# Kernel tuning notes

Hardware: AMD Instinct MI355X
Metric: run time of the kernel (lower is better)

The kernel has to match this reference:

```python
import jax, jax.numpy as jnp
import numpy as np

B, N, D, H = 1, 4096, 1024, 16
HD = D // H  # head_dim = 64


def setup_inputs() -> dict:
    key = jax.random.key(0)
    ks = jax.random.split(key, 5)
    s = 0.02
    return {
        "x": jax.random.normal(ks[0], (B, N, D), dtype=jnp.float32),
        "Wq": jax.random.normal(ks[1], (D, D), dtype=jnp.float32) * s,
        "Wk": jax.random.normal(ks[2], (D, D), dtype=jnp.float32) * s,
        "Wv": jax.random.normal(ks[3], (D, D), dtype=jnp.float32) * s,
        "Wo": jax.random.normal(ks[4], (D, D), dtype=jnp.float32) * s,
        "bo": jnp.zeros((D,), dtype=jnp.float32),
    }


def reference(x, Wq, Wk, Wv, Wo, bo):
    b, n, d = x.shape
    # QKV projections -> [b, h, n, hd]
    def proj(W):
        return jnp.einsum("bnd,de->bne", x, W).reshape(b, n, H, HD).transpose(0, 2, 1, 3)
    q, k, v = proj(Wq), proj(Wk), proj(Wv)
    # Scores [b, h, n, n] with causal mask (matches masked_fill with triu(diag=1))
    scores = jnp.einsum("bhqd,bhkd->bhqk", q, k)
    causal = jnp.tril(jnp.ones((n, n), dtype=bool))
    scores = jnp.where(causal, scores, -jnp.inf)
    attn = jax.nn.softmax(scores / jnp.sqrt(jnp.float32(HD)), axis=-1)
    # dropout p=0.0 -> identity
    ctx = jnp.einsum("bhqk,bhkd->bhqd", attn, v)
    ctx = ctx.transpose(0, 2, 1, 3).reshape(b, n, d)
    return jnp.einsum("bnd,de->bne", ctx, Wo) + bo
```

## Files before the change

### kernel.cpp

```cpp
#include <hip/hip_runtime.h>


#define N_TOK 4096
#define DMODEL 1024
#define NH 16
#define HDIM 64

typedef __bf16 bf16x8 __attribute__((ext_vector_type(8)));
typedef __bf16 bf16x2v __attribute__((ext_vector_type(2)));
typedef short short4v __attribute__((ext_vector_type(4)));
typedef unsigned int uint2v __attribute__((ext_vector_type(2)));
typedef float f32x4 __attribute__((ext_vector_type(4)));

__device__ __forceinline__ unsigned short f2bf(float f) {
  unsigned u = __builtin_bit_cast(unsigned, f);
  u += 0x7FFFu + ((u >> 16) & 1u);
  return (unsigned short)(u >> 16);
}

__device__ __forceinline__ float bf2f(unsigned short u) {
  unsigned x = (unsigned)u << 16;
  return __builtin_bit_cast(float, x);
}

__device__ __forceinline__ unsigned pack2bf(float f0, float f1) {
  unsigned a = __builtin_bit_cast(unsigned, f0);
  unsigned b = __builtin_bit_cast(unsigned, f1);
  a += 0x7FFFu + ((a >> 16) & 1u);
  b += 0x7FFFu + ((b >> 16) & 1u);
  return (a >> 16) | (b & 0xFFFF0000u);
}

__device__ __forceinline__ unsigned packpk(float f0, float f1) {
#if defined(__HIP_DEVICE_COMPILE__) && __has_builtin(__builtin_amdgcn_cvt_pk_bf16_f32)
  bf16x2v r = __builtin_amdgcn_cvt_pk_bf16_f32(f0, f1);
  return __builtin_bit_cast(unsigned, r);
#else
  return pack2bf(f0, f1);
#endif
}

__device__ __forceinline__ float fast_exp2(float x) {
#if defined(__HIP_DEVICE_COMPILE__)
#if __has_builtin(__builtin_amdgcn_exp2f)
  return __builtin_amdgcn_exp2f(x);
#else
  float r;
  asm("v_exp_f32 %0, %1" : "=v"(r) : "v"(x));
  return r;
#endif
#else
  return exp2f(x);
#endif
}

__device__ __forceinline__ f32x4 mfma16x16x16(short4v a, short4v b, f32x4 c) {
#if defined(__HIP_DEVICE_COMPILE__)
#if __has_builtin(__builtin_amdgcn_mfma_f32_16x16x16bf16_1k)
  return __builtin_amdgcn_mfma_f32_16x16x16bf16_1k(a, b, c, 0, 0, 0);
#else
  asm volatile("v_mfma_f32_16x16x16_bf16 %0, %1, %2, %0\n\ts_nop 7\n\ts_nop 1"
               : "+v"(c) : "v"(a), "v"(b));
  return c;
#endif
#else
  return c;
#endif
}

__device__ __forceinline__ void gll16(const unsigned short* g, unsigned short* l) {
#if defined(__HIP_DEVICE_COMPILE__)
  __builtin_amdgcn_global_load_lds((const __attribute__((address_space(1))) void*)g,
                                   (__attribute__((address_space(3))) void*)l, 16, 0, 0);
#endif
}

__global__ __launch_bounds__(256) void prep_kernel(
    const float* __restrict__ x, unsigned short* __restrict__ xb,
    const float* __restrict__ Wq, const float* __restrict__ Wk,
    const float* __restrict__ Wv, const float* __restrict__ Wo,
    unsigned short* __restrict__ Wqt, unsigned short* __restrict__ Wkt,
    unsigned short* __restrict__ Wvt, unsigned short* __restrict__ Wot) {
  const int bx = blockIdx.x;
  if (bx < 4096) {
    const int i = (bx * 256 + threadIdx.x) * 4;
    float4 v = *(const float4*)(x + i);
    ushort4 o;
    o.x = f2bf(v.x); o.y = f2bf(v.y); o.z = f2bf(v.z); o.w = f2bf(v.w);
    *(ushort4*)(xb + i) = o;
    return;
  }
  __shared__ float t[32][33];
  const int r = bx - 4096;
  const int z = r >> 10, rem = r & 1023;
  const int by = rem >> 5, bxx = rem & 31;
  const float* src;
  unsigned short* dst;
  switch (z) {
    case 0: src = Wq; dst = Wqt; break;
    case 1: src = Wk; dst = Wkt; break;
    case 2: src = Wv; dst = Wvt; break;
    default: src = Wo; dst = Wot; break;
  }
  const int tx = threadIdx.x & 31, ty = threadIdx.x >> 5;
  const int xx = bxx * 32 + tx;
  const int y0 = by * 32;
#pragma unroll
  for (int i = 0; i < 32; i += 8) t[ty + i][tx] = src[(y0 + ty + i) * DMODEL + xx];
  __syncthreads();
  const int ox = by * 32 + tx;
  const int oy0 = bxx * 32;
#pragma unroll
  for (int i = 0; i < 32; i += 8) dst[(oy0 + ty + i) * DMODEL + ox] = f2bf(t[tx][ty + i]);
}

__global__ __launch_bounds__(256) void gemm_qkv_kernel(
    const unsigned short* __restrict__ xb,
    const unsigned short* __restrict__ Wqt, const unsigned short* __restrict__ Wkt,
    const unsigned short* __restrict__ Wvt,
    unsigned short* __restrict__ Qg, unsigned short* __restrict__ Kg,
    unsigned short* __restrict__ Vtg) {
  __shared__ unsigned short As[128 * 32];
  __shared__ unsigned short Bs[128 * 32];
  __shared__ unsigned short Tt[64 * 132];
  const int z = blockIdx.z;
  const unsigned short* Bmat = (z == 0) ? Wqt : ((z == 1) ? Wkt : Wvt);
  const int tid = threadIdx.x, lane = tid & 63, wv = tid >> 6;
  const int quad = lane >> 4, l15 = lane & 15;
  const int wm = wv >> 1, wn = wv & 1;
  const int tm0 = blockIdx.y * 128, tn0 = blockIdx.x * 128;
  const int lrow = lane >> 2, lcol = (lane & 3) * 8;
  const f32x4 zero4 = {0.f, 0.f, 0.f, 0.f};
  f32x4 acc[4][4];
#pragma unroll
  for (int i = 0; i < 4; ++i)
#pragma unroll
    for (int j = 0; j < 4; ++j) acc[i][j] = zero4;

  for (int kb = 0; kb < DMODEL; kb += 32) {
#pragma unroll
    for (int r = 0; r < 2; ++r) {
      const int row0 = r * 64 + wv * 16;
      gll16(&xb[(tm0 + row0 + lrow) * DMODEL + kb + lcol], &As[row0 * 32]);
      gll16(&Bmat[(tn0 + row0 + lrow) * DMODEL + kb + lcol], &Bs[row0 * 32]);
    }
    __syncthreads();
    bf16x8 af[4], bfr[4];
#pragma unroll
    for (int i = 0; i < 4; ++i) {
      af[i]  = *(const bf16x8*)&As[(wm * 64 + i * 16 + l15) * 32 + quad * 8];
      bfr[i] = *(const bf16x8*)&Bs[(wn * 64 + i * 16 + l15) * 32 + quad * 8];
    }
#pragma unroll
    for (int mt = 0; mt < 4; ++mt)
#pragma unroll
      for (int nt = 0; nt < 4; ++nt)
        acc[mt][nt] = __builtin_amdgcn_mfma_f32_16x16x32_bf16(af[mt], bfr[nt], acc[mt][nt], 0, 0, 0);
    __syncthreads();
  }

  const float qs = 0.125f * 1.44269504088896f;
  if (z < 2) {
#pragma unroll
    for (int mt = 0; mt < 4; ++mt)
#pragma unroll
      for (int nt = 0; nt < 4; ++nt)
#pragma unroll
        for (int r = 0; r < 4; ++r) {
          const int row = tm0 + wm * 64 + mt * 16 + quad * 4 + r;
          const int col = tn0 + wn * 64 + nt * 16 + l15;
          const float v = acc[mt][nt][r];
          const int hh = col >> 6, hd = col & 63;
          if (z == 0) Qg[(hh * N_TOK + row) * HDIM + hd] = f2bf(v * qs);
          else        Kg[(hh * N_TOK + row) * HDIM + hd] = f2bf(v);
        }
  } else {
#pragma unroll 1
    for (int p = 0; p < 2; ++p) {
      if (wn == p) {
#pragma unroll
        for (int mt = 0; mt < 4; ++mt)
#pragma unroll
          for (int nt = 0; nt < 4; ++nt) {
            const int c = nt * 16 + l15;
#pragma unroll
            for (int r = 0; r < 4; ++r)
              Tt[c * 132 + wm * 64 + mt * 16 + quad * 4 + r] = f2bf(acc[mt][nt][r]);
          }
      }
      __syncthreads();
      const int c = tid >> 2, seg = tid & 3;
      const int hh = (tn0 + p * 64) >> 6;
      unsigned short* dst = Vtg + hh * (HDIM * N_TOK) + c * N_TOK + tm0 + seg * 32;
      const unsigned short* srcp = &Tt[c * 132 + seg * 32];
#pragma unroll
      for (int j = 0; j < 4; ++j)
        *(uint4*)(dst + j * 8) = *(const uint4*)(srcp + j * 8);
      __syncthreads();
    }
  }
}

#define TRW 68

__device__ static const unsigned char T_TAB[80] = {
    7, 14, 15, 15, 21, 22, 22, 23, 23, 23, 28, 29, 29, 30, 30, 30, 31, 31, 31, 31,
    6, 12, 13, 13, 14, 18, 19, 19, 20, 20, 20, 21, 21, 22, 24, 25, 25, 26, 26, 26,
    27, 27, 27, 27, 28, 28, 28, 29, 29, 30,
    5, 10, 11, 11, 12, 16, 16, 17, 17, 17, 18, 18, 19, 24, 24, 24, 25, 25, 26,
    4, 8, 9, 9, 10, 16,
    3, 8,
    2,
    1,
    0};
__device__ static const unsigned char G_TAB[80] = {
    0, 0, 0, 1, 0, 0, 1, 0, 1, 2, 0, 0, 1, 0, 1, 2, 0, 1, 2, 3,
    0, 0, 0, 1, 1, 0, 0, 1, 0, 1, 2, 1, 2, 2, 0, 0, 1, 0, 1, 2,
    0, 1, 2, 3, 1, 2, 3, 2, 3, 3,
    0, 0, 0, 1, 1, 0, 1, 0, 1, 2, 1, 2, 2, 1, 2, 3, 2, 3, 3,
    0, 0, 0, 1, 1, 2,
    0, 1,
    0,
    0,
    0};
__device__ static const unsigned char PS_TAB[32] = {
    0, 0, 0, 0, 0, 0, 0, 0,
    0, 2, 4, 6, 8, 10, 12, 14,
    16, 19, 22, 25, 28, 31, 34, 37,
    40, 44, 48, 52, 56, 60, 64, 68};

__device__ __forceinline__ unsigned short* part_slot_ptr(
    unsigned short* poA, unsigned short* poB, int slot) {
  return (slot < 384) ? poA + (size_t)slot * 8192
                      : poB + (size_t)(slot - 384) * 8192;
}

__device__ __forceinline__ void stage_kv(
    const unsigned short* __restrict__ Kh, const unsigned short* __restrict__ Vh,
    int kv0, char* buf, int wv, int lane) {
  unsigned short* Ksb = (unsigned short*)buf;
  unsigned short* Vsb = (unsigned short*)(buf + 8192);
  const int r8 = lane >> 3, g = lane & 7;
  const int sw = ((g ^ r8) * 8);
#pragma unroll
  for (int i = 0; i < 2; ++i) {
    const int row = wv * 16 + i * 8;
    gll16(&Kh[(kv0 + row + r8) * HDIM + sw], &Ksb[row * 64]);
    gll16(&Vh[(row + r8) * N_TOK + kv0 + sw], &Vsb[row * 64]);
  }
}

template <bool MASKED>
__device__ __forceinline__ void attn_step(
    int kvs, int qw, int quad, int l15,
    const unsigned short* __restrict__ Ks, const unsigned short* __restrict__ Vs,
    const bf16x8 (&qf)[2][2], f32x4 (&o)[2][4], float (&l_)[2]) {
  const f32x4 zero4 = {0.f, 0.f, 0.f, 0.f};
  const int s = l15 & 7;
  f32x4 c[2][4];
#pragma unroll
  for (int mt = 0; mt < 4; ++mt) {
    const unsigned short* kp = &Ks[(mt * 16 + l15) * 64];
    const int g0 = (quad ^ s) * 8;
    const bf16x8 kf0 = *(const bf16x8*)(kp + g0);
    const bf16x8 kf1 = *(const bf16x8*)(kp + (g0 ^ 32));
#pragma unroll
    for (int qt = 0; qt < 2; ++qt) {
      c[qt][mt] = __builtin_amdgcn_mfma_f32_16x16x32_bf16(kf0, qf[qt][0], zero4, 0, 0, 0);
      c[qt][mt] = __builtin_amdgcn_mfma_f32_16x16x32_bf16(kf1, qf[qt][1], c[qt][mt], 0, 0, 0);
    }
  }
  short4v pb[2][4];
#pragma unroll
  for (int qt = 0; qt < 2; ++qt) {
    const int q = qw + qt * 16 + l15;
    float ls = 0.f;
#pragma unroll
    for (int mt = 0; mt < 4; ++mt) {
      float p[4];
#pragma unroll
      for (int r = 0; r < 4; ++r) {
        float v = c[qt][mt][r];
        if (MASKED) v = ((kvs + mt * 16 + quad * 4 + r) <= q) ? v : -3e38f;
        p[r] = fast_exp2(v);
      }
      ls += (p[0] + p[1]) + (p[2] + p[3]);
      uint2v w;
      w.x = packpk(p[0], p[1]);
      w.y = packpk(p[2], p[3]);
      pb[qt][mt] = __builtin_bit_cast(short4v, w);
    }
    l_[qt] += ls;
  }
#pragma unroll
  for (int mt = 0; mt < 4; ++mt)
#pragma unroll
    for (int dt = 0; dt < 4; ++dt) {
      const int gv = (((2 * mt + (quad >> 1)) ^ s) * 8) + (quad & 1) * 4;
      const short4v vfx = *(const short4v*)&Vs[(dt * 16 + l15) * 64 + gv];
      o[0][dt] = mfma16x16x16(vfx, pb[0][mt], o[0][dt]);
      o[1][dt] = mfma16x16x16(vfx, pb[1][mt], o[1][dt]);
    }
}

__global__ __launch_bounds__(256, 4) void attn_kernel(
    const unsigned short* __restrict__ Qg, const unsigned short* __restrict__ Kg,
    const unsigned short* __restrict__ Vtg, unsigned short* __restrict__ ctx,
    unsigned short* __restrict__ part_oA, unsigned short* __restrict__ part_oB,
    float* __restrict__ part_l) {
  __shared__ __align__(16) char smem[32768];
  const int tid = threadIdx.x, lane = tid & 63, wv = tid >> 6;
  const int quad = lane >> 4, l15 = lane & 15;

  const int xcd = blockIdx.x & 7;
  const int iblk = blockIdx.x >> 3;
  const int h = (xcd << 1) | (iblk & 1);
  const int u = iblk >> 1;
  const int t = T_TAB[u], g = G_TAB[u];
  const int ng = (t >> 3) + 1;
  const int tp1 = t + 1;
  const int gbase = tp1 / ng;
  const int grem = tp1 - gbase * ng;
  const int s0 = g * gbase + (g < grem ? g : grem);
  const int cnt = gbase + (g < grem ? 1 : 0);
  const int mlen = 2 * cnt;
  const bool multi = (t >= 8);
  const int qb = t * 128, qw = qb + wv * 32;

  const unsigned short* Qh = Qg + h * N_TOK * HDIM;
  const unsigned short* Kh = Kg + h * N_TOK * HDIM;
  const unsigned short* Vh = Vtg + h * HDIM * N_TOK;

  bf16x8 qf[2][2];
#pragma unroll
  for (int qt = 0; qt < 2; ++qt)
#pragma unroll
    for (int hh = 0; hh < 2; ++hh)
      qf[qt][hh] = *(const bf16x8*)&Qh[(qw + qt * 16 + l15) * HDIM + hh * 32 + quad * 8];

  const f32x4 zero4 = {0.f, 0.f, 0.f, 0.f};
  f32x4 o[2][4];
#pragma unroll
  for (int qt = 0; qt < 2; ++qt)
#pragma unroll
    for (int dt = 0; dt < 4; ++dt) o[qt][dt] = zero4;
  float l_[2] = {0.f, 0.f};

  const int kvbase = s0 << 7;
  stage_kv(Kh, Vh, kvbase, smem, wv, lane);
  stage_kv(Kh, Vh, kvbase + 64, smem + 16384, wv, lane);
  int cur = 0;
#pragma unroll 1
  for (int mc = 0; mc < mlen; ++mc) {
    const int kv0 = kvbase + mc * 64;
    if (mc + 1 < mlen) asm volatile("s_waitcnt vmcnt(4)" ::: "memory");
    else               asm volatile("s_waitcnt vmcnt(0)" ::: "memory");
    __builtin_amdgcn_s_barrier();
    const unsigned short* Ksb = (const unsigned short*)(smem + cur * 16384);
    const unsigned short* Vsb = (const unsigned short*)(smem + cur * 16384 + 8192);
    if (kv0 <= qw + 31) {
      __builtin_amdgcn_s_setprio(1);
      if (kv0 + 63 <= qw)
        attn_step<false>(kv0, qw, quad, l15, Ksb, Vsb, qf, o, l_);
      else
        attn_step<true>(kv0, qw, quad, l15, Ksb, Vsb, qf, o, l_);
      __builtin_amdgcn_s_setprio(0);
    }
    if (mc + 2 < mlen) {
      __builtin_amdgcn_s_barrier();
      stage_kv(Kh, Vh, kv0 + 128, smem + cur * 16384, wv, lane);
    }
    cur ^= 1;
  }
  __syncthreads();

  float* Tr = (float*)(smem + wv * (16 * TRW * 4));
  const int tq = lane >> 2, seg = lane & 3;
  if (!multi) {
#pragma unroll
    for (int qt = 0; qt < 2; ++qt) {
      float l = l_[qt];
      l += __shfl_xor(l, 16, 64);
      l += __shfl_xor(l, 32, 64);
      const float inv = 1.0f / l;
#pragma unroll
      for (int dt = 0; dt < 4; ++dt) {
        f32x4 v = o[qt][dt] * inv;
        *(f32x4*)&Tr[l15 * TRW + dt * 16 + quad * 4] = v;
      }
      unsigned short* dst = &ctx[(qb + wv * 32 + qt * 16 + tq) * DMODEL + h * HDIM + seg * 16];
      const float* src = &Tr[tq * TRW + seg * 16];
#pragma unroll
      for (int j = 0; j < 2; ++j) {
        const float* s8 = src + j * 8;
        uint4 w;
        w.x = pack2bf(s8[0], s8[1]);
        w.y = pack2bf(s8[2], s8[3]);
        w.z = pack2bf(s8[4], s8[5]);
        w.w = pack2bf(s8[6], s8[7]);
        *(uint4*)(dst + j * 8) = w;
      }
    }
  } else {
    const int slot = h * 72 + PS_TAB[t] + g;
    unsigned short* pobase = part_slot_ptr(part_oA, part_oB, slot);
#pragma unroll
    for (int qt = 0; qt < 2; ++qt) {
      float l = l_[qt];
      l += __shfl_xor(l, 16, 64);
      l += __shfl_xor(l, 32, 64);
      if (quad == 0) part_l[slot * 128 + wv * 32 + qt * 16 + l15] = l;
#pragma unroll
      for (int dt = 0; dt < 4; ++dt)
        *(f32x4*)&Tr[l15 * TRW + dt * 16 + quad * 4] = o[qt][dt];
      unsigned short* dst = pobase + (wv * 32 + qt * 16 + tq) * 64 + seg * 16;
      const float* src = &Tr[tq * TRW + seg * 16];
#pragma unroll
      for (int j = 0; j < 2; ++j) {
        const float* s8 = src + j * 8;
        uint4 w;
        w.x = pack2bf(s8[0], s8[1]);
        w.y = pack2bf(s8[2], s8[3]);
        w.z = pack2bf(s8[4], s8[5]);
        w.w = pack2bf(s8[6], s8[7]);
        *(uint4*)(dst + j * 8) = w;
      }
    }
  }
}

__global__ __launch_bounds__(256) void merge_kernel(
    unsigned short* __restrict__ part_oA, unsigned short* __restrict__ part_oB,
    const float* __restrict__ part_l, unsigned short* __restrict__ ctx) {
  const int b = blockIdx.x;
  const int h = b / 24, tt = b - h * 24;
  const int t = tt + 8;
  const int ng = (t >> 3) + 1;
  const int tid = threadIdx.x;
  const int q = tid >> 1, half = tid & 1;
  const int slot0 = h * 72 + PS_TAB[t];
  float l = 0.f;
  for (int g = 0; g < ng; ++g) l += part_l[(slot0 + g) * 128 + q];
  const float inv = 1.0f / l;
  unsigned short* dst = &ctx[(t * 128 + q) * DMODEL + h * HDIM + half * 32];
#pragma unroll
  for (int j = 0; j < 4; ++j) {
    float acc[8] = {0.f, 0.f, 0.f, 0.f, 0.f, 0.f, 0.f, 0.f};
    for (int g = 0; g < ng; ++g) {
      const unsigned short* po = part_slot_ptr(part_oA, part_oB, slot0 + g);
      const uint4 w = *(const uint4*)(po + q * 64 + half * 32 + j * 8);
      const unsigned short* us = (const unsigned short*)&w;
#pragma unroll
      for (int e = 0; e < 8; ++e) acc[e] += bf2f(us[e]);
    }
    uint4 w;
    w.x = pack2bf(acc[0] * inv, acc[1] * inv);
    w.y = pack2bf(acc[2] * inv, acc[3] * inv);
    w.z = pack2bf(acc[4] * inv, acc[5] * inv);
    w.w = pack2bf(acc[6] * inv, acc[7] * inv);
    *(uint4*)(dst + j * 8) = w;
  }
}

__global__ __launch_bounds__(256) void gemm_out_kernel(
    const unsigned short* __restrict__ ctxb, const unsigned short* __restrict__ Wot,
    const float* __restrict__ bo, float* __restrict__ out) {
  __shared__ unsigned short As[128 * 32];
  __shared__ unsigned short Bs[64 * 32];
  const int tid = threadIdx.x, lane = tid & 63, wv = tid >> 6;
  const int quad = lane >> 4, l15 = lane & 15;
  const int wm = wv >> 1, wn = wv & 1;
  const int tm0 = blockIdx.y * 128, tn0 = blockIdx.x * 64;
  const int lrow = lane >> 2, lcol = (lane & 3) * 8;
  const f32x4 zero4 = {0.f, 0.f, 0.f, 0.f};
  f32x4 acc[4][2];
#pragma unroll
  for (int i = 0; i < 4; ++i)
#pragma unroll
    for (int j = 0; j < 2; ++j) acc[i][j] = zero4;

  for (int kb = 0; kb < DMODEL; kb += 32) {
    {
      const int ra = wv * 32;
      gll16(&ctxb[(tm0 + ra + lrow) * DMODEL + kb + lcol], &As[ra * 32]);
      gll16(&ctxb[(tm0 + ra + 16 + lrow) * DMODEL + kb + lcol], &As[(ra + 16) * 32]);
      const int rb = wv * 16;
      gll16(&Wot[(tn0 + rb + lrow) * DMODEL + kb + lcol], &Bs[rb * 32]);
    }
    __syncthreads();
    bf16x8 af[4], bfr[2];
#pragma unroll
    for (int i = 0; i < 4; ++i)
      af[i] = *(const bf16x8*)&As[(wm * 64 + i * 16 + l15) * 32 + quad * 8];
#pragma unroll
    for (int j = 0; j < 2; ++j)
      bfr[j] = *(const bf16x8*)&Bs[(wn * 32 + j * 16 + l15) * 32 + quad * 8];
#pragma unroll
    for (int mt = 0; mt < 4; ++mt)
#pragma unroll
      for (int nt = 0; nt < 2; ++nt)
        acc[mt][nt] = __builtin_amdgcn_mfma_f32_16x16x32_bf16(af[mt], bfr[nt], acc[mt][nt], 0, 0, 0);
    __syncthreads();
  }
#pragma unroll
  for (int mt = 0; mt < 4; ++mt)
#pragma unroll
    for (int nt = 0; nt < 2; ++nt)
#pragma unroll
      for (int r = 0; r < 4; ++r) {
        const int row = tm0 + wm * 64 + mt * 16 + quad * 4 + r;
        const int col = tn0 + wn * 32 + nt * 16 + l15;
        out[row * DMODEL + col] = acc[mt][nt][r] + bo[col];
      }
}

extern "C" void kernel_launch(void* const* d_in, const int* in_sizes, int n_in,
                              void* d_out, int out_size, void* d_ws, size_t ws_size,
                              hipStream_t stream) {
  const float* x  = (const float*)d_in[0];
  const float* Wq = (const float*)d_in[1];
  const float* Wk = (const float*)d_in[2];
  const float* Wv = (const float*)d_in[3];
  const float* Wo = (const float*)d_in[4];
  const float* bo = (const float*)d_in[5];
  float* out = (float*)d_out;

  char* ws = (char*)d_ws;
  unsigned short* xb  = (unsigned short*)(ws);
  unsigned short* Wqt = (unsigned short*)(ws + 8388608);
  unsigned short* Wkt = (unsigned short*)(ws + 8388608 + 2097152);
  unsigned short* Wvt = (unsigned short*)(ws + 8388608 + 2 * 2097152);
  unsigned short* Wot = (unsigned short*)(ws + 8388608 + 3 * 2097152);
  unsigned short* Qg  = (unsigned short*)(ws + 16777216);
  unsigned short* Kg  = (unsigned short*)(ws + 25165824);
  unsigned short* Vtg = (unsigned short*)(ws + 33554432);
  unsigned short* ctx = xb;
  unsigned short* part_oA = (unsigned short*)(ws + 8388608);
  unsigned short* part_oB = (unsigned short*)(ws + 41943040);
  float* part_l = (float*)(ws + 54525952);

  prep_kernel<<<8192, 256, 0, stream>>>(x, xb, Wq, Wk, Wv, Wo, Wqt, Wkt, Wvt, Wot);
  gemm_qkv_kernel<<<dim3(DMODEL / 128, N_TOK / 128, 3), 256, 0, stream>>>(xb, Wqt, Wkt, Wvt, Qg, Kg, Vtg);
  attn_kernel<<<1280, 256, 0, stream>>>(Qg, Kg, Vtg, ctx, part_oA, part_oB, part_l);
  merge_kernel<<<384, 256, 0, stream>>>(part_oA, part_oB, part_l, ctx);
  gemm_out_kernel<<<dim3(DMODEL / 64, N_TOK / 128), 256, 0, stream>>>(ctx, Wot, bo, out);
}
```

Before: 221.2 us.

## Double-buffer LDS tiles in QKV and output GEMMs with async prefetch

Both projection GEMMs now keep two LDS stages and issue global-to-LDS loads for the tile two steps ahead, waiting with partial vmcnt counts instead of a full syncthreads each iteration. This aims to hide global load latency behind MFMA work in the K loop. It also enlarges the attention kernel's shared allocation, which may lower occupancy there, and it relies on hand-written waitcnt values matching the compiler's load counts.

```diff
diff --git a/kernel.cpp b/kernel.cpp
--- a/kernel.cpp
+++ b/kernel.cpp
@@ -120,9 +120,7 @@
     const unsigned short* __restrict__ Wvt,
     unsigned short* __restrict__ Qg, unsigned short* __restrict__ Kg,
     unsigned short* __restrict__ Vtg) {
-  __shared__ unsigned short As[128 * 32];
-  __shared__ unsigned short Bs[128 * 32];
-  __shared__ unsigned short Tt[64 * 132];
+  __shared__ __align__(16) char smem[32768];
   const int z = blockIdx.z;
   const unsigned short* Bmat = (z == 0) ? Wqt : ((z == 1) ? Wkt : Wvt);
   const int tid = threadIdx.x, lane = tid & 63, wv = tid >> 6;
@@ -137,14 +135,27 @@
 #pragma unroll
     for (int j = 0; j < 4; ++j) acc[i][j] = zero4;
 
-  for (int kb = 0; kb < DMODEL; kb += 32) {
+  auto stage = [&](int kb, int b) {
+    unsigned short* As = (unsigned short*)(smem + b * 16384);
+    unsigned short* Bs = (unsigned short*)(smem + b * 16384 + 8192);
 #pragma unroll
     for (int r = 0; r < 2; ++r) {
       const int row0 = r * 64 + wv * 16;
       gll16(&xb[(tm0 + row0 + lrow) * DMODEL + kb + lcol], &As[row0 * 32]);
       gll16(&Bmat[(tn0 + row0 + lrow) * DMODEL + kb + lcol], &Bs[row0 * 32]);
     }
-    __syncthreads();
+  };
+
+  stage(0, 0);
+  stage(32, 1);
+  int cur = 0;
+#pragma unroll 1
+  for (int kb = 0; kb < DMODEL; kb += 32) {
+    if (kb + 32 < DMODEL) asm volatile("s_waitcnt vmcnt(4)" ::: "memory");
+    else                  asm volatile("s_waitcnt vmcnt(0)" ::: "memory");
+    __builtin_amdgcn_s_barrier();
+    const unsigned short* As = (const unsigned short*)(smem + cur * 16384);
+    const unsigned short* Bs = (const unsigned short*)(smem + cur * 16384 + 8192);
     bf16x8 af[4], bfr[4];
 #pragma unroll
     for (int i = 0; i < 4; ++i) {
@@ -156,8 +167,13 @@
 #pragma unroll
       for (int nt = 0; nt < 4; ++nt)
         acc[mt][nt] = __builtin_amdgcn_mfma_f32_16x16x32_bf16(af[mt], bfr[nt], acc[mt][nt], 0, 0, 0);
-    __syncthreads();
-  }
+    if (kb + 64 < DMODEL) {
+      __builtin_amdgcn_s_barrier();
+      stage(kb + 64, cur);
+    }
+    cur ^= 1;
+  }
+  __syncthreads();
 
   const float qs = 0.125f * 1.44269504088896f;
   if (z < 2) {
@@ -175,6 +191,7 @@
           else        Kg[(hh * N_TOK + row) * HDIM + hd] = f2bf(v);
         }
   } else {
+    unsigned short* Tt = (unsigned short*)smem;
 #pragma unroll 1
     for (int p = 0; p < 2; ++p) {
       if (wn == p) {
@@ -308,7 +325,7 @@
     const unsigned short* __restrict__ Vtg, unsigned short* __restrict__ ctx,
     unsigned short* __restrict__ part_oA, unsigned short* __restrict__ part_oB,
     float* __restrict__ part_l) {
-  __shared__ __align__(16) char smem[32768];
+  __shared__ __align__(16) char smem[34816];
   const int tid = threadIdx.x, lane = tid & 63, wv = tid >> 6;
   const int quad = lane >> 4, l15 = lane & 15;
 
@@ -465,8 +482,7 @@
 __global__ __launch_bounds__(256) void gemm_out_kernel(
     const unsigned short* __restrict__ ctxb, const unsigned short* __restrict__ Wot,
     const float* __restrict__ bo, float* __restrict__ out) {
-  __shared__ unsigned short As[128 * 32];
-  __shared__ unsigned short Bs[64 * 32];
+  __shared__ __align__(16) char smem[24576];
   const int tid = threadIdx.x, lane = tid & 63, wv = tid >> 6;
   const int quad = lane >> 4, l15 = lane & 15;
   const int wm = wv >> 1, wn = wv & 1;
@@ -479,15 +495,25 @@
 #pragma unroll
     for (int j = 0; j < 2; ++j) acc[i][j] = zero4;
 
+  auto stage = [&](int kb, int b) {
+    unsigned short* As = (unsigned short*)(smem + b * 8192);
+    unsigned short* Bs = (unsigned short*)(smem + 16384 + b * 4096);
+    const int ra = wv * 32;
+    gll16(&ctxb[(tm0 + ra + lrow) * DMODEL + kb + lcol], &As[ra * 32]);
+    gll16(&ctxb[(tm0 + ra + 16 + lrow) * DMODEL + kb + lcol], &As[(ra + 16) * 32]);
+    const int rb = wv * 16;
+    gll16(&Wot[(tn0 + rb + lrow) * DMODEL + kb + lcol], &Bs[rb * 32]);
+  };
+  stage(0, 0);
+  stage(32, 1);
+  int cur = 0;
+#pragma unroll 1
   for (int kb = 0; kb < DMODEL; kb += 32) {
-    {
-      const int ra = wv * 32;
-      gll16(&ctxb[(tm0 + ra + lrow) * DMODEL + kb + lcol], &As[ra * 32]);
-      gll16(&ctxb[(tm0 + ra + 16 + lrow) * DMODEL + kb + lcol], &As[(ra + 16) * 32]);
-      const int rb = wv * 16;
-      gll16(&Wot[(tn0 + rb + lrow) * DMODEL + kb + lcol], &Bs[rb * 32]);
-    }
-    __syncthreads();
+    if (kb + 32 < DMODEL) asm volatile("s_waitcnt vmcnt(3)" ::: "memory");
+    else                  asm volatile("s_waitcnt vmcnt(0)" ::: "memory");
+    __builtin_amdgcn_s_barrier();
+    const unsigned short* As = (const unsigned short*)(smem + cur * 8192);
+    const unsigned short* Bs = (const unsigned short*)(smem + 16384 + cur * 4096);
     bf16x8 af[4], bfr[2];
 #pragma unroll
     for (int i = 0; i < 4; ++i)
@@ -500,7 +526,11 @@
 #pragma unroll
       for (int nt = 0; nt < 2; ++nt)
         acc[mt][nt] = __builtin_amdgcn_mfma_f32_16x16x32_bf16(af[mt], bfr[nt], acc[mt][nt], 0, 0, 0);
-    __syncthreads();
+    if (kb + 64 < DMODEL) {
+      __builtin_amdgcn_s_barrier();
+      stage(kb + 64, cur);
+    }
+    cur ^= 1;
   }
 #pragma unroll
   for (int mt = 0; mt < 4; ++mt)
```

Measured after the change: 206.2 us (median of 2 runs). -6.8%, faster.
